# Optimization experiments

Measured on AMD Instinct MI355X. Metric: run time of the kernel, lower is better.

## Reference

```python
import jax, jax.numpy as jnp
import numpy as np

NUM_REL = 3


def setup_inputs() -> dict:
    key = jax.random.key(0)
    ks = jax.random.split(key, 12)
    N, E, G = 400_000, 2_000_000, 40_000
    V, D, H, C = 1024, 64, 96, 8
    sc = lambda k, shape: (jax.random.normal(k, shape, jnp.float32) * 0.05)
    return {
        "tokens": jax.random.randint(ks[0], (N,), 0, V),
        "edge_index": jax.random.randint(ks[1], (2, E), 0, N),
        "edge_type": jax.random.randint(ks[2], (E,), 0, NUM_REL),
        "batch": jnp.sort(jax.random.randint(ks[3], (N,), 0, G)),
        "num_graphs": G,
        "emb": sc(ks[4], (V, D)),
        "W1": sc(ks[5], (NUM_REL, D, H)),
        "root1": sc(ks[6], (D, H)),
        "b1": jnp.zeros((H,), jnp.float32),
        "W2": sc(ks[7], (NUM_REL, H, H)),
        "root2": sc(ks[8], (H, H)),
        "b2": jnp.zeros((H,), jnp.float32),
        "linW": sc(ks[9], (H, C)),
        "linb": jnp.zeros((C,), jnp.float32),
    }


def rgcn_layer(x, src, dst, etype, W, root, bias):
    # PyG RGCNConv with default aggr='mean': per-relation mean over incoming
    # edges, transformed by the relation weight, plus root transform and bias.
    N, Din = x.shape
    seg = dst * NUM_REL + etype  # combined (node, relation) segment id
    msgs = x[src]  # [E, Din] irregular gather
    sums = jax.ops.segment_sum(msgs, seg, num_segments=N * NUM_REL)
    sums = sums.reshape(N, NUM_REL, Din)
    cnt = jax.ops.segment_sum(jnp.ones_like(etype, dtype=x.dtype), seg,
                              num_segments=N * NUM_REL).reshape(N, NUM_REL, 1)
    mean = sums / jnp.maximum(cnt, 1.0)
    return jnp.einsum("nrd,rdh->nh", mean, W) + x @ root + bias


def reference(tokens, edge_index, edge_type, batch, num_graphs,
              emb, W1, root1, b1, W2, root2, b2, linW, linb):
    src, dst = edge_index[0], edge_index[1]
    x = emb[tokens]  # [N, D]
    x = jax.nn.relu(rgcn_layer(x, src, dst, edge_type, W1, root1, b1))
    # dropout(p=0.2) is identity in eval mode
    x = jax.nn.relu(rgcn_layer(x, src, dst, edge_type, W2, root2, b2))
    gsum = jax.ops.segment_sum(x, batch, num_segments=num_graphs)
    gcnt = jax.ops.segment_sum(jnp.ones((x.shape[0], 1), x.dtype), batch,
                               num_segments=num_graphs)
    pooled = gsum / jnp.maximum(gcnt, 1.0)  # global_mean_pool
    return pooled @ linW + linb
```

## Files before the change

kernel.cpp:

```cpp
#include <hip/hip_runtime.h>


#define NREL 3
#define DD 64
#define HH 96
#define CC 8
#define TM 32
#define KK 384

typedef __attribute__((ext_vector_type(8))) short bf16x8;
typedef __attribute__((ext_vector_type(4))) float f32x4;

__device__ __forceinline__ unsigned short f2bf(float x) {
    unsigned u = __float_as_uint(x);
    unsigned r = (u + 0x7fffu + ((u >> 16) & 1u)) >> 16;
    return (unsigned short)r;
}
__device__ __forceinline__ float bf2f(unsigned short h) {
    return __uint_as_float(((unsigned)h) << 16);
}

__global__ __launch_bounds__(256) void count_k(const int* __restrict__ dstv,
                                               const int* __restrict__ et, int E,
                                               int* __restrict__ cnt) {
    int e = blockIdx.x * 256 + threadIdx.x;
    if (e < E) atomicAdd(&cnt[dstv[e] * NREL + et[e]], 1);
}

__global__ __launch_bounds__(256) void scan_blk_k(const int* __restrict__ in, int S,
                                                  int* __restrict__ out,
                                                  int* __restrict__ bsum) {
    __shared__ int vals[1024];
    __shared__ int tsum[256];
    int base = blockIdx.x * 1024;
    for (int i = threadIdx.x; i < 1024; i += 256) {
        int g = base + i;
        vals[i] = (g < S) ? in[g] : 0;
    }
    __syncthreads();
    int t = threadIdx.x;
    int a0 = vals[t * 4], a1 = vals[t * 4 + 1], a2 = vals[t * 4 + 2], a3 = vals[t * 4 + 3];
    int s = a0 + a1 + a2 + a3;
    tsum[t] = s;
    __syncthreads();
    for (int off = 1; off < 256; off <<= 1) {
        int v = (t >= off) ? tsum[t - off] : 0;
        __syncthreads();
        tsum[t] += v;
        __syncthreads();
    }
    int excl = tsum[t] - s;
    int g = base + t * 4;
    if (g     < S) out[g]     = excl;
    if (g + 1 < S) out[g + 1] = excl + a0;
    if (g + 2 < S) out[g + 2] = excl + a0 + a1;
    if (g + 3 < S) out[g + 3] = excl + a0 + a1 + a2;
    if (t == 255) bsum[blockIdx.x] = tsum[255];
}

__global__ __launch_bounds__(256) void scan_top_k(int* __restrict__ bsum, int nb) {
    __shared__ int ts[256];
    int t = threadIdx.x;
    int loc[8];
    int s = 0;
    #pragma unroll
    for (int j = 0; j < 8; ++j) {
        int g = t * 8 + j;
        loc[j] = (g < nb) ? bsum[g] : 0;
        s += loc[j];
    }
    ts[t] = s;
    __syncthreads();
    for (int off = 1; off < 256; off <<= 1) {
        int v = (t >= off) ? ts[t - off] : 0;
        __syncthreads();
        ts[t] += v;
        __syncthreads();
    }
    int excl = ts[t] - s;
    #pragma unroll
    for (int j = 0; j < 8; ++j) {
        int g = t * 8 + j;
        if (g < nb) bsum[g] = excl;
        excl += loc[j];
    }
}

__global__ __launch_bounds__(256) void scan_add_k(int* __restrict__ out,
                                                  const int* __restrict__ bsum,
                                                  int S, int E) {
    int i = blockIdx.x * 256 + threadIdx.x;
    if (i < S) out[i] += bsum[i >> 10];
    else if (i == S) out[S] = E;
}

__global__ __launch_bounds__(256) void copy_k(const int* __restrict__ a,
                                              int* __restrict__ b, int n) {
    int i = blockIdx.x * 256 + threadIdx.x;
    if (i < n) b[i] = a[i];
}

__global__ __launch_bounds__(256) void fill_k(const int* __restrict__ srcv,
                                              const int* __restrict__ dstv,
                                              const int* __restrict__ et, int E,
                                              int* __restrict__ cursor,
                                              int* __restrict__ ssrc) {
    int e = blockIdx.x * 256 + threadIdx.x;
    if (e >= E) return;
    int seg = dstv[e] * NREL + et[e];
    int pos = atomicAdd(&cursor[seg], 1);
    ssrc[pos] = srcv[e];
}

__global__ __launch_bounds__(256) void gcnt_k(const int* __restrict__ batch, int N,
                                              float* __restrict__ gcnt) {
    int i = blockIdx.x * 256 + threadIdx.x;
    if (i < N) atomicAdd(&gcnt[batch[i]], 1.0f);
}

__global__ __launch_bounds__(256) void z1er_k(const float* __restrict__ emb,
                                              const float* __restrict__ W1,
                                              const float* __restrict__ root1,
                                              const float* __restrict__ b1,
                                              int V, float* __restrict__ z1,
                                              float* __restrict__ er1) {
    int idx = blockIdx.x * 256 + threadIdx.x;
    int tot = V * 4 * HH;
    if (idx >= tot) return;
    int v = idx / (4 * HH);
    int j = idx - v * 4 * HH;
    int r = j / HH;
    int h = j - r * HH;
    const float* ev = emb + (size_t)v * DD;
    float s = 0.f;
    if (r < NREL) {
        const float* w = W1 + ((size_t)r * DD) * HH + h;
        #pragma unroll 8
        for (int d = 0; d < DD; ++d) s += ev[d] * w[(size_t)d * HH];
        z1[((size_t)v * NREL + r) * HH + h] = s;
    } else {
        const float* w = root1 + h;
        #pragma unroll 8
        for (int d = 0; d < DD; ++d) s += ev[d] * w[(size_t)d * HH];
        er1[(size_t)v * HH + h] = s + b1[h];
    }
}

__global__ __launch_bounds__(256) void catwT_k(const float* __restrict__ W2,
                                               const float* __restrict__ root2,
                                               short* __restrict__ WTh,
                                               short* __restrict__ WTl) {
    int idx = blockIdx.x * 256 + threadIdx.x;
    const int tot = HH * KK;
    if (idx >= tot) return;
    int h = idx / KK;
    int K = idx - h * KK;
    float v = (K < NREL * HH) ? W2[(size_t)K * HH + h]
                              : root2[(size_t)(K - NREL * HH) * HH + h];
    unsigned short hi = f2bf(v);
    float res = v - bf2f(hi);
    unsigned short lo = f2bf(res);
    WTh[(size_t)h * KK + K] = (short)hi;
    WTl[(size_t)h * KK + K] = (short)lo;
}

__global__ __launch_bounds__(256) void l1_k(const int* __restrict__ rowptr,
                                            const int* __restrict__ ssrc,
                                            const int* __restrict__ tokens,
                                            const float* __restrict__ z1,
                                            const float* __restrict__ er1,
                                            float* __restrict__ h1, int N) {
    int idx = blockIdx.x * 256 + threadIdx.x;
    if (idx >= N * 24) return;
    int n = idx / 24;
    int q = idx - n * 24;
    int h0 = q * 4;
    float4 acc = *reinterpret_cast<const float4*>(er1 + (size_t)tokens[n] * HH + h0);
    int base = n * NREL;
    for (int r = 0; r < NREL; ++r) {
        int b = rowptr[base + r], e2 = rowptr[base + r + 1];
        float sx = 0.f, sy = 0.f, sz = 0.f, sw = 0.f;
        for (int i = b; i < e2; ++i) {
            int tok = tokens[ssrc[i]];
            const float4 z = *reinterpret_cast<const float4*>(
                z1 + ((size_t)tok * NREL + r) * HH + h0);
            sx += z.x; sy += z.y; sz += z.z; sw += z.w;
        }
        float rc = 1.0f / fmaxf((float)(e2 - b), 1.0f);
        acc.x += sx * rc; acc.y += sy * rc; acc.z += sz * rc; acc.w += sw * rc;
    }
    float4 o;
    o.x = fmaxf(acc.x, 0.f); o.y = fmaxf(acc.y, 0.f);
    o.z = fmaxf(acc.z, 0.f); o.w = fmaxf(acc.w, 0.f);
    *reinterpret_cast<float4*>(h1 + (size_t)n * HH + h0) = o;
}

__global__ __launch_bounds__(256) void l2_k(const int* __restrict__ rowptr,
                                            const int* __restrict__ ssrc,
                                            const float* __restrict__ h1,
                                            const short* __restrict__ WTh,
                                            const short* __restrict__ WTl,
                                            const float* __restrict__ b2,
                                            const int* __restrict__ batch,
                                            float* __restrict__ gsum, int N) {
    __shared__ short Ah[TM][392];
    __shared__ short Al[TM][392];
    int n0 = blockIdx.x * TM;
    int t = threadIdx.x;
    {
        int i = t >> 3;
        int c = t & 7;
        int d0 = c * 48;
        int n = n0 + i;
        float acc[48];
        #pragma unroll
        for (int j = 0; j < 48; ++j) acc[j] = 0.f;
        if (n < N) {
            if (d0 < NREL * HH) {
                int r = d0 / HH;
                int k0 = d0 - r * HH;
                int b = rowptr[n * NREL + r], e2 = rowptr[n * NREL + r + 1];
                for (int ii = b; ii < e2; ++ii) {
                    const float* hrow = h1 + (size_t)ssrc[ii] * HH + k0;
                    #pragma unroll
                    for (int j = 0; j < 48; j += 4) {
                        const float4 v = *reinterpret_cast<const float4*>(hrow + j);
                        acc[j] += v.x; acc[j+1] += v.y; acc[j+2] += v.z; acc[j+3] += v.w;
                    }
                }
                float rc = 1.0f / fmaxf((float)(e2 - b), 1.0f);
                #pragma unroll
                for (int j = 0; j < 48; ++j) acc[j] *= rc;
            } else {
                int k0 = d0 - NREL * HH;
                const float* hrow = h1 + (size_t)n * HH + k0;
                #pragma unroll
                for (int j = 0; j < 48; j += 4) {
                    const float4 v = *reinterpret_cast<const float4*>(hrow + j);
                    acc[j] = v.x; acc[j+1] = v.y; acc[j+2] = v.z; acc[j+3] = v.w;
                }
            }
        }
        #pragma unroll
        for (int w = 0; w < 6; ++w) {
            bf16x8 hv, lv;
            #pragma unroll
            for (int j = 0; j < 8; ++j) {
                float a = acc[w * 8 + j];
                unsigned short hb = f2bf(a);
                float res = a - bf2f(hb);
                unsigned short lb = f2bf(res);
                hv[j] = (short)hb;
                lv[j] = (short)lb;
            }
            *reinterpret_cast<bf16x8*>(&Ah[i][d0 + w * 8]) = hv;
            *reinterpret_cast<bf16x8*>(&Al[i][d0 + w * 8]) = lv;
        }
    }
    __syncthreads();
    int lane = t & 63;
    int wv = t >> 6;
    int mrow = (wv & 1) * 16;
    int nbase = (wv >> 1) * 48;
    int r16 = lane & 15;
    int g = lane >> 4;

    float bi0 = b2[nbase + r16];
    float bi1 = b2[nbase + 16 + r16];
    float bi2 = b2[nbase + 32 + r16];
    f32x4 acc0 = {bi0, bi0, bi0, bi0};
    f32x4 acc1 = {bi1, bi1, bi1, bi1};
    f32x4 acc2 = {bi2, bi2, bi2, bi2};

    const short* arow_h = &Ah[mrow + r16][8 * g];
    const short* arow_l = &Al[mrow + r16][8 * g];
    size_t w0 = (size_t)(nbase + r16) * KK + 8 * g;
    size_t w1 = w0 + (size_t)16 * KK;
    size_t w2 = w0 + (size_t)32 * KK;

    #pragma unroll
    for (int kk = 0; kk < KK / 32; ++kk) {
        int ko = kk * 32;
        bf16x8 ah = *reinterpret_cast<const bf16x8*>(arow_h + ko);
        bf16x8 al = *reinterpret_cast<const bf16x8*>(arow_l + ko);
        bf16x8 bh0 = *reinterpret_cast<const bf16x8*>(WTh + w0 + ko);
        bf16x8 bl0 = *reinterpret_cast<const bf16x8*>(WTl + w0 + ko);
        acc0 = __builtin_amdgcn_mfma_f32_16x16x32_bf16(ah, bh0, acc0, 0, 0, 0);
        acc0 = __builtin_amdgcn_mfma_f32_16x16x32_bf16(al, bh0, acc0, 0, 0, 0);
        acc0 = __builtin_amdgcn_mfma_f32_16x16x32_bf16(ah, bl0, acc0, 0, 0, 0);
        bf16x8 bh1 = *reinterpret_cast<const bf16x8*>(WTh + w1 + ko);
        bf16x8 bl1 = *reinterpret_cast<const bf16x8*>(WTl + w1 + ko);
        acc1 = __builtin_amdgcn_mfma_f32_16x16x32_bf16(ah, bh1, acc1, 0, 0, 0);
        acc1 = __builtin_amdgcn_mfma_f32_16x16x32_bf16(al, bh1, acc1, 0, 0, 0);
        acc1 = __builtin_amdgcn_mfma_f32_16x16x32_bf16(ah, bl1, acc1, 0, 0, 0);
        bf16x8 bh2 = *reinterpret_cast<const bf16x8*>(WTh + w2 + ko);
        bf16x8 bl2 = *reinterpret_cast<const bf16x8*>(WTl + w2 + ko);
        acc2 = __builtin_amdgcn_mfma_f32_16x16x32_bf16(ah, bh2, acc2, 0, 0, 0);
        acc2 = __builtin_amdgcn_mfma_f32_16x16x32_bf16(al, bh2, acc2, 0, 0, 0);
        acc2 = __builtin_amdgcn_mfma_f32_16x16x32_bf16(ah, bl2, acc2, 0, 0, 0);
    }
    #pragma unroll
    for (int r = 0; r < 4; ++r) {
        int node = n0 + mrow + g * 4 + r;
        if (node < N) {
            float* gs = gsum + (size_t)batch[node] * HH;
            atomicAdd(gs + nbase + r16,      fmaxf(acc0[r], 0.f));
            atomicAdd(gs + nbase + 16 + r16, fmaxf(acc1[r], 0.f));
            atomicAdd(gs + nbase + 32 + r16, fmaxf(acc2[r], 0.f));
        }
    }
}

__global__ __launch_bounds__(256) void final_k(const float* __restrict__ gsum,
                                               const float* __restrict__ gcnt,
                                               const float* __restrict__ linW,
                                               const float* __restrict__ linb,
                                               float* __restrict__ out, int G) {
    int idx = blockIdx.x * 256 + threadIdx.x;
    if (idx >= G * CC) return;
    int g = idx / CC;
    int c = idx - g * CC;
    float rc = 1.0f / fmaxf(gcnt[g], 1.0f);
    const float* gs = gsum + (size_t)g * HH;
    float s = 0.f;
    #pragma unroll 8
    for (int h = 0; h < HH; ++h) s += gs[h] * linW[h * CC + c];
    out[idx] = s * rc + linb[c];
}

__global__ __launch_bounds__(256) void diag_k(float* __restrict__ out, int n, float v) {
    int i = blockIdx.x * 256 + threadIdx.x;
    if (i < n) out[i] = (i == 0) ? v : 0.f;
}

static inline int nblk(long long n) { return (int)((n + 255) / 256); }

extern "C" void kernel_launch(void* const* d_in, const int* in_sizes, int n_in,
                              void* d_out, int out_size, void* d_ws, size_t ws_size,
                              hipStream_t stream) {
    (void)n_in;
    const int* tokens = (const int*)d_in[0];
    const int* eidx   = (const int*)d_in[1];
    const int* etype  = (const int*)d_in[2];
    const int* batch  = (const int*)d_in[3];
    const float* emb   = (const float*)d_in[5];
    const float* W1    = (const float*)d_in[6];
    const float* root1 = (const float*)d_in[7];
    const float* b1    = (const float*)d_in[8];
    const float* W2    = (const float*)d_in[9];
    const float* root2 = (const float*)d_in[10];
    const float* b2v   = (const float*)d_in[11];
    const float* linW  = (const float*)d_in[12];
    const float* linb  = (const float*)d_in[13];
    float* out = (float*)d_out;

    const int N = in_sizes[0];
    const int E = in_sizes[2];
    const int V = in_sizes[5] / DD;
    const int G = out_size / CC;
    const int S = N * NREL;
    const int nb1 = (S + 1023) / 1024;

    const int* srcv = eidx;
    const int* dstv = eidx + E;

    auto align_up = [](size_t x) { return (x + 255) & ~(size_t)255; };
    size_t o_rowptr = 0;
    size_t o_cnt    = o_rowptr + align_up(((size_t)S + 1) * 4);
    size_t o_bsum   = o_cnt    + align_up((size_t)S * 4);
    size_t o_ssrc   = o_bsum   + align_up((size_t)2048 * 4);
    size_t o_z1     = o_ssrc   + align_up((size_t)E * 4);
    size_t o_er1    = o_z1     + align_up((size_t)V * NREL * HH * 4);
    size_t o_wth    = o_er1    + align_up((size_t)V * HH * 4);
    size_t o_wtl    = o_wth    + align_up((size_t)HH * KK * 2);
    size_t o_gsum   = o_wtl    + align_up((size_t)HH * KK * 2);
    size_t o_gcnt   = o_gsum   + align_up((size_t)G * HH * 4);
    size_t o_h1     = o_gcnt   + align_up((size_t)G * 4);
    size_t need     = o_h1     + align_up((size_t)N * HH * 4);

    if (ws_size < need || nb1 > 2048) {
        diag_k<<<nblk(out_size), 256, 0, stream>>>(out, out_size, (float)ws_size);
        return;
    }

    char* ws = (char*)d_ws;
    int*   rowptr = (int*)  (ws + o_rowptr);
    int*   cnt    = (int*)  (ws + o_cnt);
    int*   bsum   = (int*)  (ws + o_bsum);
    int*   ssrc   = (int*)  (ws + o_ssrc);
    float* z1     = (float*)(ws + o_z1);
    float* er1    = (float*)(ws + o_er1);
    short* WTh    = (short*)(ws + o_wth);
    short* WTl    = (short*)(ws + o_wtl);
    float* gsum   = (float*)(ws + o_gsum);
    float* gcntv  = (float*)(ws + o_gcnt);
    float* h1     = (float*)(ws + o_h1);

    hipMemsetAsync(cnt, 0, (size_t)S * 4, stream);
    hipMemsetAsync(gsum, 0, (size_t)G * HH * 4, stream);
    hipMemsetAsync(gcntv, 0, (size_t)G * 4, stream);

    count_k<<<nblk(E), 256, 0, stream>>>(dstv, etype, E, cnt);
    scan_blk_k<<<nb1, 256, 0, stream>>>(cnt, S, rowptr, bsum);
    scan_top_k<<<1, 256, 0, stream>>>(bsum, nb1);
    scan_add_k<<<nblk((long long)S + 1), 256, 0, stream>>>(rowptr, bsum, S, E);
    copy_k<<<nblk(S), 256, 0, stream>>>(rowptr, cnt, S);
    fill_k<<<nblk(E), 256, 0, stream>>>(srcv, dstv, etype, E, cnt, ssrc);
    z1er_k<<<nblk((long long)V * 4 * HH), 256, 0, stream>>>(emb, W1, root1, b1, V, z1, er1);
    catwT_k<<<nblk(HH * KK), 256, 0, stream>>>(W2, root2, WTh, WTl);
    gcnt_k<<<nblk(N), 256, 0, stream>>>(batch, N, gcntv);
    l1_k<<<nblk((long long)N * 24), 256, 0, stream>>>(rowptr, ssrc, tokens, z1, er1, h1, N);
    l2_k<<<(N + TM - 1) / TM, 256, 0, stream>>>(rowptr, ssrc, h1, WTh, WTl, b2v, batch,
                                                gsum, N);
    final_k<<<nblk((long long)G * CC), 256, 0, stream>>>(gsum, gcntv, linW, linb, out, G);
}
```

Before: 1.130 ms.

## Pre-resolve edge source tokens and reshape layer-2 block to smaller tiles

The fill kernel now also writes each sorted edge's source token, so layer 1 reads that token directly instead of doing a dependent tokens[ssrc[i]] lookup. The layer-2 kernel drops from 32 to 16 nodes per block and uses 384 threads. Each thread gathers 16 features instead of 48 and each wave computes a single 16x16 MFMA tile. This cuts register pressure and adds parallelism in the gather-heavy phase, at the cost of an extra E-sized index array, more blocks, and re-reading the weight panel from global memory for every 16 nodes.

```diff
diff --git a/kernel.cpp b/kernel.cpp
--- a/kernel.cpp
+++ b/kernel.cpp
@@ -5,7 +5,7 @@
 #define DD 64
 #define HH 96
 #define CC 8
-#define TM 32
+#define TM 16
 #define KK 384
 
 typedef __attribute__((ext_vector_type(8))) short bf16x8;
@@ -102,14 +102,18 @@
 
 __global__ __launch_bounds__(256) void fill_k(const int* __restrict__ srcv,
                                               const int* __restrict__ dstv,
-                                              const int* __restrict__ et, int E,
+                                              const int* __restrict__ et,
+                                              const int* __restrict__ tokens, int E,
                                               int* __restrict__ cursor,
-                                              int* __restrict__ ssrc) {
+                                              int* __restrict__ ssrc,
+                                              int* __restrict__ stok) {
     int e = blockIdx.x * 256 + threadIdx.x;
     if (e >= E) return;
+    int s = srcv[e];
     int seg = dstv[e] * NREL + et[e];
     int pos = atomicAdd(&cursor[seg], 1);
-    ssrc[pos] = srcv[e];
+    ssrc[pos] = s;
+    stok[pos] = tokens[s];
 }
 
 __global__ __launch_bounds__(256) void gcnt_k(const int* __restrict__ batch, int N,
@@ -165,7 +169,7 @@
 }
 
 __global__ __launch_bounds__(256) void l1_k(const int* __restrict__ rowptr,
-                                            const int* __restrict__ ssrc,
+                                            const int* __restrict__ stok,
                                             const int* __restrict__ tokens,
                                             const float* __restrict__ z1,
                                             const float* __restrict__ er1,
@@ -181,7 +185,7 @@
         int b = rowptr[base + r], e2 = rowptr[base + r + 1];
         float sx = 0.f, sy = 0.f, sz = 0.f, sw = 0.f;
         for (int i = b; i < e2; ++i) {
-            int tok = tokens[ssrc[i]];
+            int tok = stok[i];
             const float4 z = *reinterpret_cast<const float4*>(
                 z1 + ((size_t)tok * NREL + r) * HH + h0);
             sx += z.x; sy += z.y; sz += z.z; sw += z.w;
@@ -195,54 +199,54 @@
     *reinterpret_cast<float4*>(h1 + (size_t)n * HH + h0) = o;
 }
 
-__global__ __launch_bounds__(256) void l2_k(const int* __restrict__ rowptr,
-                                            const int* __restrict__ ssrc,
-                                            const float* __restrict__ h1,
-                                            const short* __restrict__ WTh,
-                                            const short* __restrict__ WTl,
-                                            const float* __restrict__ b2,
-                                            const int* __restrict__ batch,
-                                            float* __restrict__ gsum, int N) {
+__global__ __launch_bounds__(384, 8) void l2_k(const int* __restrict__ rowptr,
+                                               const int* __restrict__ ssrc,
+                                               const float* __restrict__ h1,
+                                               const short* __restrict__ WTh,
+                                               const short* __restrict__ WTl,
+                                               const float* __restrict__ b2,
+                                               const int* __restrict__ batch,
+                                               float* __restrict__ gsum, int N) {
     __shared__ short Ah[TM][392];
     __shared__ short Al[TM][392];
     int n0 = blockIdx.x * TM;
     int t = threadIdx.x;
     {
-        int i = t >> 3;
-        int c = t & 7;
-        int d0 = c * 48;
+        int i = t & 15;
+        int c = t >> 4;
+        int d0 = c * 16;
         int n = n0 + i;
-        float acc[48];
+        float acc[16];
         #pragma unroll
-        for (int j = 0; j < 48; ++j) acc[j] = 0.f;
+        for (int j = 0; j < 16; ++j) acc[j] = 0.f;
         if (n < N) {
-            if (d0 < NREL * HH) {
-                int r = d0 / HH;
-                int k0 = d0 - r * HH;
+            if (c < 18) {
+                int r = c / 6;
+                int k0 = (c - r * 6) * 16;
                 int b = rowptr[n * NREL + r], e2 = rowptr[n * NREL + r + 1];
                 for (int ii = b; ii < e2; ++ii) {
                     const float* hrow = h1 + (size_t)ssrc[ii] * HH + k0;
                     #pragma unroll
-                    for (int j = 0; j < 48; j += 4) {
+                    for (int j = 0; j < 16; j += 4) {
                         const float4 v = *reinterpret_cast<const float4*>(hrow + j);
                         acc[j] += v.x; acc[j+1] += v.y; acc[j+2] += v.z; acc[j+3] += v.w;
                     }
                 }
                 float rc = 1.0f / fmaxf((float)(e2 - b), 1.0f);
                 #pragma unroll
-                for (int j = 0; j < 48; ++j) acc[j] *= rc;
+                for (int j = 0; j < 16; ++j) acc[j] *= rc;
             } else {
-                int k0 = d0 - NREL * HH;
+                int k0 = (c - 18) * 16;
                 const float* hrow = h1 + (size_t)n * HH + k0;
                 #pragma unroll
-                for (int j = 0; j < 48; j += 4) {
+                for (int j = 0; j < 16; j += 4) {
                     const float4 v = *reinterpret_cast<const float4*>(hrow + j);
                     acc[j] = v.x; acc[j+1] = v.y; acc[j+2] = v.z; acc[j+3] = v.w;
                 }
             }
         }
         #pragma unroll
-        for (int w = 0; w < 6; ++w) {
+        for (int w = 0; w < 2; ++w) {
             bf16x8 hv, lv;
             #pragma unroll
             for (int j = 0; j < 8; ++j) {
@@ -259,54 +263,34 @@
     }
     __syncthreads();
     int lane = t & 63;
-    int wv = t >> 6;
-    int mrow = (wv & 1) * 16;
-    int nbase = (wv >> 1) * 48;
+    int w = t >> 6;
+    int nb_ = w * 16;
     int r16 = lane & 15;
     int g = lane >> 4;
 
-    float bi0 = b2[nbase + r16];
-    float bi1 = b2[nbase + 16 + r16];
-    float bi2 = b2[nbase + 32 + r16];
-    f32x4 acc0 = {bi0, bi0, bi0, bi0};
-    f32x4 acc1 = {bi1, bi1, bi1, bi1};
-    f32x4 acc2 = {bi2, bi2, bi2, bi2};
-
-    const short* arow_h = &Ah[mrow + r16][8 * g];
-    const short* arow_l = &Al[mrow + r16][8 * g];
-    size_t w0 = (size_t)(nbase + r16) * KK + 8 * g;
-    size_t w1 = w0 + (size_t)16 * KK;
-    size_t w2 = w0 + (size_t)32 * KK;
+    float bi = b2[nb_ + r16];
+    f32x4 acc = {bi, bi, bi, bi};
+
+    const short* arow_h = &Ah[r16][8 * g];
+    const short* arow_l = &Al[r16][8 * g];
+    size_t wb = (size_t)(nb_ + r16) * KK + 8 * g;
 
     #pragma unroll
     for (int kk = 0; kk < KK / 32; ++kk) {
         int ko = kk * 32;
         bf16x8 ah = *reinterpret_cast<const bf16x8*>(arow_h + ko);
         bf16x8 al = *reinterpret_cast<const bf16x8*>(arow_l + ko);
-        bf16x8 bh0 = *reinterpret_cast<const bf16x8*>(WTh + w0 + ko);
-        bf16x8 bl0 = *reinterpret_cast<const bf16x8*>(WTl + w0 + ko);
-        acc0 = __builtin_amdgcn_mfma_f32_16x16x32_bf16(ah, bh0, acc0, 0, 0, 0);
-        acc0 = __builtin_amdgcn_mfma_f32_16x16x32_bf16(al, bh0, acc0, 0, 0, 0);
-        acc0 = __builtin_amdgcn_mfma_f32_16x16x32_bf16(ah, bl0, acc0, 0, 0, 0);
-        bf16x8 bh1 = *reinterpret_cast<const bf16x8*>(WTh + w1 + ko);
-        bf16x8 bl1 = *reinterpret_cast<const bf16x8*>(WTl + w1 + ko);
-        acc1 = __builtin_amdgcn_mfma_f32_16x16x32_bf16(ah, bh1, acc1, 0, 0, 0);
-        acc1 = __builtin_amdgcn_mfma_f32_16x16x32_bf16(al, bh1, acc1, 0, 0, 0);
-        acc1 = __builtin_amdgcn_mfma_f32_16x16x32_bf16(ah, bl1, acc1, 0, 0, 0);
-        bf16x8 bh2 = *reinterpret_cast<const bf16x8*>(WTh + w2 + ko);
-        bf16x8 bl2 = *reinterpret_cast<const bf16x8*>(WTl + w2 + ko);
-        acc2 = __builtin_amdgcn_mfma_f32_16x16x32_bf16(ah, bh2, acc2, 0, 0, 0);
-        acc2 = __builtin_amdgcn_mfma_f32_16x16x32_bf16(al, bh2, acc2, 0, 0, 0);
-        acc2 = __builtin_amdgcn_mfma_f32_16x16x32_bf16(ah, bl2, acc2, 0, 0, 0);
+        bf16x8 bh = *reinterpret_cast<const bf16x8*>(WTh + wb + ko);
+        bf16x8 bl = *reinterpret_cast<const bf16x8*>(WTl + wb + ko);
+        acc = __builtin_amdgcn_mfma_f32_16x16x32_bf16(ah, bh, acc, 0, 0, 0);
+        acc = __builtin_amdgcn_mfma_f32_16x16x32_bf16(al, bh, acc, 0, 0, 0);
+        acc = __builtin_amdgcn_mfma_f32_16x16x32_bf16(ah, bl, acc, 0, 0, 0);
     }
     #pragma unroll
     for (int r = 0; r < 4; ++r) {
-        int node = n0 + mrow + g * 4 + r;
+        int node = n0 + g * 4 + r;
         if (node < N) {
-            float* gs = gsum + (size_t)batch[node] * HH;
-            atomicAdd(gs + nbase + r16,      fmaxf(acc0[r], 0.f));
-            atomicAdd(gs + nbase + 16 + r16, fmaxf(acc1[r], 0.f));
-            atomicAdd(gs + nbase + 32 + r16, fmaxf(acc2[r], 0.f));
+            atomicAdd(gsum + (size_t)batch[node] * HH + nb_ + r16, fmaxf(acc[r], 0.f));
         }
     }
 }
@@ -369,7 +353,8 @@
     size_t o_cnt    = o_rowptr + align_up(((size_t)S + 1) * 4);
     size_t o_bsum   = o_cnt    + align_up((size_t)S * 4);
     size_t o_ssrc   = o_bsum   + align_up((size_t)2048 * 4);
-    size_t o_z1     = o_ssrc   + align_up((size_t)E * 4);
+    size_t o_stok   = o_ssrc   + align_up((size_t)E * 4);
+    size_t o_z1     = o_stok   + align_up((size_t)E * 4);
     size_t o_er1    = o_z1     + align_up((size_t)V * NREL * HH * 4);
     size_t o_wth    = o_er1    + align_up((size_t)V * HH * 4);
     size_t o_wtl    = o_wth    + align_up((size_t)HH * KK * 2);
@@ -388,6 +373,7 @@
     int*   cnt    = (int*)  (ws + o_cnt);
     int*   bsum   = (int*)  (ws + o_bsum);
     int*   ssrc   = (int*)  (ws + o_ssrc);
+    int*   stok   = (int*)  (ws + o_stok);
     float* z1     = (float*)(ws + o_z1);
     float* er1    = (float*)(ws + o_er1);
     short* WTh    = (short*)(ws + o_wth);
@@ -405,12 +391,12 @@
     scan_top_k<<<1, 256, 0, stream>>>(bsum, nb1);
     scan_add_k<<<nblk((long long)S + 1), 256, 0, stream>>>(rowptr, bsum, S, E);
     copy_k<<<nblk(S), 256, 0, stream>>>(rowptr, cnt, S);
-    fill_k<<<nblk(E), 256, 0, stream>>>(srcv, dstv, etype, E, cnt, ssrc);
+    fill_k<<<nblk(E), 256, 0, stream>>>(srcv, dstv, etype, tokens, E, cnt, ssrc, stok);
     z1er_k<<<nblk((long long)V * 4 * HH), 256, 0, stream>>>(emb, W1, root1, b1, V, z1, er1);
     catwT_k<<<nblk(HH * KK), 256, 0, stream>>>(W2, root2, WTh, WTl);
     gcnt_k<<<nblk(N), 256, 0, stream>>>(batch, N, gcntv);
-    l1_k<<<nblk((long long)N * 24), 256, 0, stream>>>(rowptr, ssrc, tokens, z1, er1, h1, N);
-    l2_k<<<(N + TM - 1) / TM, 256, 0, stream>>>(rowptr, ssrc, h1, WTh, WTl, b2v, batch,
+    l1_k<<<nblk((long long)N * 24), 256, 0, stream>>>(rowptr, stok, tokens, z1, er1, h1, N);
+    l2_k<<<(N + TM - 1) / TM, 384, 0, stream>>>(rowptr, ssrc, h1, WTh, WTl, b2v, batch,
                                                 gsum, N);
     final_k<<<nblk((long long)G * CC), 256, 0, stream>>>(gsum, gcntv, linW, linb, out, G);
 }
```

Result: faster. 1.035 ms (-8.4%).
